# Performance work log

Measured on AMD Instinct MI355X. Metric: run time of the kernel, lower is better.

Reference implementation:

```python
import jax, jax.numpy as jnp
import numpy as np

N, E, D, IN_DIM, NUM_CLASSES, G, L = 50000, 800000, 128, 128, 10, 64, 3
BN_EPS = 1e-5


def _bn(h, gamma, beta, mean, var):
    # inference-mode batchnorm with running stats
    return (h - mean) * jax.lax.rsqrt(var + BN_EPS) * gamma + beta


def setup_inputs() -> dict:
    key = jax.random.key(0)
    ks = jax.random.split(key, 24)
    s = 0.02
    x = jax.random.normal(ks[0], (N, IN_DIM), dtype=jnp.float32)
    c_2 = jax.random.randint(ks[1], (E,), 0, N)
    u_2 = jax.random.randint(ks[2], (E,), 0, N)
    batch = jnp.sort(jax.random.randint(ks[3], (N,), 0, G))
    inp = {
        "x": x, "c_2": c_2, "u_2": u_2, "batch": batch,
        "We": jax.random.normal(ks[4], (IN_DIM, D)) * s,
        "be": jnp.zeros((D,), jnp.float32),
        # per-layer GIN MLP: Linear(d,2d) -> BN(2d) -> ReLU -> Linear(2d,d)
        "W1": jax.random.normal(ks[5], (L, D, 2 * D)) * s,
        "b1": jnp.zeros((L, 2 * D), jnp.float32),
        "g1": jnp.ones((L, 2 * D), jnp.float32),
        "bt1": jnp.zeros((L, 2 * D), jnp.float32),
        "m1": jax.random.normal(ks[6], (L, 2 * D)) * 0.1,
        "v1": jax.random.uniform(ks[7], (L, 2 * D), minval=0.5, maxval=1.5),
        "W2": jax.random.normal(ks[8], (L, 2 * D, D)) * s,
        "b2": jnp.zeros((L, D), jnp.float32),
        # post-conv BatchNorm(d)
        "g2": jnp.ones((L, D), jnp.float32),
        "bt2": jnp.zeros((L, D), jnp.float32),
        "m2": jax.random.normal(ks[9], (L, D)) * 0.1,
        "v2": jax.random.uniform(ks[10], (L, D), minval=0.5, maxval=1.5),
        # readout: Linear(d,d) -> ReLU -> (dropout off) -> Linear(d,num_classes)
        "Wr1": jax.random.normal(ks[11], (D, D)) * s,
        "br1": jnp.zeros((D,), jnp.float32),
        "Wr2": jax.random.normal(ks[12], (D, NUM_CLASSES)) * s,
        "br2": jnp.zeros((NUM_CLASSES,), jnp.float32),
    }
    return inp


def reference(x, c_2, u_2, batch, We, be, W1, b1, g1, bt1, m1, v1,
              W2, b2, g2, bt2, m2, v2, Wr1, br1, Wr2, br2):
    h = x @ We + be  # [N, D]
    for l in range(L):
        # GINConv (eps=0): h_i <- MLP(h_i + sum_{j->i} h_j)
        agg = jax.ops.segment_sum(h[c_2], u_2, num_segments=N)  # [N, D]
        z = h + agg
        z = jax.nn.relu(_bn(z @ W1[l] + b1[l], g1[l], bt1[l], m1[l], v1[l]))
        z = z @ W2[l] + b2[l]
        h = jax.nn.relu(_bn(z, g2[l], bt2[l], m2[l], v2[l]))
        # dropout: identity in eval mode
    pooled = jax.ops.segment_sum(h, batch, num_segments=G)  # [G, D]
    out = jax.nn.relu(pooled @ Wr1 + br1) @ Wr2 + br2  # [G, num_classes]
    return out
```

## Files before the change

kernel.cpp:

```cpp
#include <hip/hip_runtime.h>

#define BN_EPS 1e-5f

typedef __attribute__((ext_vector_type(8))) short bf16x8;
typedef __attribute__((ext_vector_type(4))) float f32x4;
typedef unsigned int uint32;

__device__ __forceinline__ unsigned short f2bf(float f) {
    unsigned u = __float_as_uint(f);
    u += 0x7FFFu + ((u >> 16) & 1u);
    return (unsigned short)(u >> 16);
}
__device__ __forceinline__ float bf2f(unsigned short u) {
    return __uint_as_float((unsigned)u << 16);
}
__device__ __forceinline__ float lo_bf(uint32 u) { return __uint_as_float(u << 16); }
__device__ __forceinline__ float hi_bf(uint32 u) { return __uint_as_float(u & 0xFFFF0000u); }
__device__ __forceinline__ uint32 pack_bf(float a0, float a1) {
    return ((uint32)f2bf(a1) << 16) | (uint32)f2bf(a0);
}

__global__ void init_kernel(int* __restrict__ deg, float* __restrict__ pooled, int N, int GP) {
    int i = blockIdx.x * 256 + threadIdx.x;
    if (i < N) deg[i] = 0;
    if (i < GP) pooled[i] = 0.f;
}

__global__ void count_deg_kernel(const int* __restrict__ u, int* __restrict__ deg, int E) {
    for (int e = blockIdx.x * blockDim.x + threadIdx.x; e < E; e += gridDim.x * blockDim.x)
        atomicAdd(&deg[u[e]], 1);
}

__global__ __launch_bounds__(256) void scan_local_kernel(const int* __restrict__ cnt,
                                                         int* __restrict__ start,
                                                         int* __restrict__ partials, int n) {
    __shared__ int buf[256];
    int i = blockIdx.x * 256 + threadIdx.x;
    int v = (i < n) ? cnt[i] : 0;
    buf[threadIdx.x] = v;
    __syncthreads();
    for (int off = 1; off < 256; off <<= 1) {
        int t = (threadIdx.x >= off) ? buf[threadIdx.x - off] : 0;
        __syncthreads();
        buf[threadIdx.x] += t;
        __syncthreads();
    }
    if (i < n) start[i] = buf[threadIdx.x] - v;
    if (threadIdx.x == 255) partials[blockIdx.x] = buf[255];
}

__global__ __launch_bounds__(256) void scan_partials_kernel(int* __restrict__ partials, int nb) {
    __shared__ int buf[256];
    int v = (threadIdx.x < nb) ? partials[threadIdx.x] : 0;
    buf[threadIdx.x] = v;
    __syncthreads();
    for (int off = 1; off < 256; off <<= 1) {
        int t = (threadIdx.x >= off) ? buf[threadIdx.x - off] : 0;
        __syncthreads();
        buf[threadIdx.x] += t;
        __syncthreads();
    }
    if (threadIdx.x < nb) partials[threadIdx.x] = buf[threadIdx.x] - v;
}

__global__ __launch_bounds__(256) void scan_add_kernel(int* __restrict__ node_start,
                                                       int* __restrict__ coarse_cursor,
                                                       const int* __restrict__ partials,
                                                       int n, int total) {
    int i = blockIdx.x * 256 + threadIdx.x;
    if (i < n) {
        int v = node_start[i] + partials[blockIdx.x];
        node_start[i] = v;
        if ((i & 255) == 0) coarse_cursor[i >> 8] = v;
    } else if (i == n) {
        node_start[n] = total;
    }
}

__global__ __launch_bounds__(256) void bin_coarse_kernel(const int* __restrict__ u2,
                                                         const int* __restrict__ c2,
                                                         int* __restrict__ coarse_cursor,
                                                         int* __restrict__ buck, int E) {
    __shared__ int lcnt[256];
    __shared__ int lbase[256];
    const int tid = threadIdx.x;
    lcnt[tid] = 0;
    __syncthreads();
    const int e0 = blockIdx.x * 4096;
    int ue[16];
#pragma unroll
    for (int k = 0; k < 16; ++k) {
        int e = e0 + k * 256 + tid;
        int u = (e < E) ? u2[e] : -1;
        ue[k] = u;
        if (u >= 0) atomicAdd(&lcnt[u >> 8], 1);
    }
    __syncthreads();
    int c0 = lcnt[tid];
    lbase[tid] = c0 ? atomicAdd(&coarse_cursor[tid], c0) : 0;
    lcnt[tid] = 0;
    __syncthreads();
#pragma unroll
    for (int k = 0; k < 16; ++k) {
        int e = e0 + k * 256 + tid;
        if (e < E) {
            int u = ue[k];
            int cb = u >> 8;
            int pos = lbase[cb] + atomicAdd(&lcnt[cb], 1);
            buck[pos] = ((u & 255) << 16) | c2[e];
        }
    }
}

__global__ __launch_bounds__(256) void bin_node_kernel(const int* __restrict__ node_start,
                                                       const int* __restrict__ buck,
                                                       int* __restrict__ csr_src, int N, int E) {
    __shared__ int lcur[256];
    const int cb = blockIdx.x;
    const int tid = threadIdx.x;
    int idx = cb * 256 + tid;
    lcur[tid] = (idx < N) ? node_start[idx] : E;
    __syncthreads();
    const int s = node_start[cb * 256];
    const int t_end = node_start[min(cb * 256 + 256, N)];
    for (int e = s + tid; e < t_end; e += 256) {
        int v = buck[e];
        int pos = atomicAdd(&lcur[v >> 16], 1);
        csr_src[pos] = v & 0xFFFF;
    }
}

__global__ __launch_bounds__(256) void aggregate_kernel(const unsigned short* __restrict__ h,
                                                        const int* __restrict__ row_start,
                                                        const int* __restrict__ csr_src,
                                                        unsigned short* __restrict__ h2, int N) {
    int node = blockIdx.x * 4 + (threadIdx.x >> 6);
    int lane = threadIdx.x & 63;
    if (node >= N) return;
    const int q = lane >> 4, sl = lane & 15;

    float a0 = 0.f, a1 = 0.f, a2 = 0.f, a3 = 0.f, a4 = 0.f, a5 = 0.f, a6 = 0.f, a7 = 0.f;
    if (q == 0) {
        uint4 v = ((const uint4*)(h + (size_t)node * 128))[sl];
        a0 = lo_bf(v.x); a1 = hi_bf(v.x); a2 = lo_bf(v.y); a3 = hi_bf(v.y);
        a4 = lo_bf(v.z); a5 = hi_bf(v.z); a6 = lo_bf(v.w); a7 = hi_bf(v.w);
    }

    const int rs = row_start[node], re = row_start[node + 1];
    int e = rs;
    for (; e + 8 <= re; e += 8) {
        int s0 = csr_src[e + q];
        int s1 = csr_src[e + 4 + q];
        uint4 v = ((const uint4*)(h + (size_t)s0 * 128))[sl];
        uint4 w = ((const uint4*)(h + (size_t)s1 * 128))[sl];
        a0 += lo_bf(v.x) + lo_bf(w.x); a1 += hi_bf(v.x) + hi_bf(w.x);
        a2 += lo_bf(v.y) + lo_bf(w.y); a3 += hi_bf(v.y) + hi_bf(w.y);
        a4 += lo_bf(v.z) + lo_bf(w.z); a5 += hi_bf(v.z) + hi_bf(w.z);
        a6 += lo_bf(v.w) + lo_bf(w.w); a7 += hi_bf(v.w) + hi_bf(w.w);
    }
    for (; e + 4 <= re; e += 4) {
        int s0 = csr_src[e + q];
        uint4 v = ((const uint4*)(h + (size_t)s0 * 128))[sl];
        a0 += lo_bf(v.x); a1 += hi_bf(v.x); a2 += lo_bf(v.y); a3 += hi_bf(v.y);
        a4 += lo_bf(v.z); a5 += hi_bf(v.z); a6 += lo_bf(v.w); a7 += hi_bf(v.w);
    }
    if (q < re - e) {
        int s0 = csr_src[e + q];
        uint4 v = ((const uint4*)(h + (size_t)s0 * 128))[sl];
        a0 += lo_bf(v.x); a1 += hi_bf(v.x); a2 += lo_bf(v.y); a3 += hi_bf(v.y);
        a4 += lo_bf(v.z); a5 += hi_bf(v.z); a6 += lo_bf(v.w); a7 += hi_bf(v.w);
    }

    a0 += __shfl_xor(a0, 16, 64); a0 += __shfl_xor(a0, 32, 64);
    a1 += __shfl_xor(a1, 16, 64); a1 += __shfl_xor(a1, 32, 64);
    a2 += __shfl_xor(a2, 16, 64); a2 += __shfl_xor(a2, 32, 64);
    a3 += __shfl_xor(a3, 16, 64); a3 += __shfl_xor(a3, 32, 64);
    a4 += __shfl_xor(a4, 16, 64); a4 += __shfl_xor(a4, 32, 64);
    a5 += __shfl_xor(a5, 16, 64); a5 += __shfl_xor(a5, 32, 64);
    a6 += __shfl_xor(a6, 16, 64); a6 += __shfl_xor(a6, 32, 64);
    a7 += __shfl_xor(a7, 16, 64); a7 += __shfl_xor(a7, 32, 64);

    if (q == 0) {
        uint4 o;
        o.x = pack_bf(a0, a1); o.y = pack_bf(a2, a3);
        o.z = pack_bf(a4, a5); o.w = pack_bf(a6, a7);
        ((uint4*)(h2 + (size_t)node * 128))[sl] = o;
    }
}

__global__ void prep_kernel(const float* __restrict__ We, const float* __restrict__ W1,
                            const float* __restrict__ W2,
                            unsigned short* __restrict__ Wte,
                            unsigned short* __restrict__ Wt1,
                            unsigned short* __restrict__ Wt2,
                            const float* __restrict__ be,
                            const float* __restrict__ b1, const float* __restrict__ g1,
                            const float* __restrict__ bt1, const float* __restrict__ m1,
                            const float* __restrict__ v1,
                            const float* __restrict__ b2, const float* __restrict__ g2,
                            const float* __restrict__ bt2, const float* __restrict__ m2,
                            const float* __restrict__ v2,
                            float* __restrict__ sce, float* __restrict__ she,
                            float* __restrict__ sc1, float* __restrict__ sh1,
                            float* __restrict__ sc2, float* __restrict__ sh2, int L) {
    int y = blockIdx.y;
    int t = threadIdx.x;
    if (blockIdx.x == 0) {
        if (y == 0) {
            if (t < 128) { sce[t] = 1.f; she[t] = be[t]; }
        } else if (y <= L) {
            int o = (y - 1) * 256 + t;
            float s = g1[o] * rsqrtf(v1[o] + BN_EPS);
            sc1[o] = s;
            sh1[o] = (b1[o] - m1[o]) * s + bt1[o];
        } else {
            if (t < 128) {
                int o = (y - L - 1) * 128 + t;
                float s = g2[o] * rsqrtf(v2[o] + BN_EPS);
                sc2[o] = s;
                sh2[o] = (b2[o] - m2[o]) * s + bt2[o];
            }
        }
    }
    const float* src;
    unsigned short* dst;
    int K;
    if (y == 0)      { src = We; dst = Wte; K = 128; }
    else if (y <= L) { int l = y - 1;     src = W1 + (size_t)l * 128 * 256; dst = Wt1 + (size_t)l * 128 * 256; K = 128; }
    else             { int l = y - L - 1; src = W2 + (size_t)l * 256 * 128; dst = Wt2 + (size_t)l * 256 * 128; K = 256; }
    int idx = blockIdx.x * 256 + t;
    int OUT = 32768 / K;
    if (y == 0) { if (idx >= 128 * 128) return; OUT = 128; }
    int c = idx / K, k = idx % K;
    dst[idx] = f2bf(src[(size_t)k * OUT + c]);
}

template <int K, int OUT, bool RELU, bool A_F32>
__global__ __launch_bounds__(256) void mfma_gemm_kernel(
    const void* __restrict__ Ap, const unsigned short* __restrict__ Wt,
    const float* __restrict__ scale, const float* __restrict__ shift,
    unsigned short* __restrict__ Cout, int nrows)
{
    constexpr int NT = OUT / 16;
    constexpr int KS = K / 32;
    constexpr int CH = OUT * K / 8;
    __shared__ unsigned short WtLds[OUT * K];

    const int tid = threadIdx.x;
    {
        const float4* src = (const float4*)Wt;
#pragma unroll
        for (int i = 0; i < CH / 256; ++i) {
            int c = tid + i * 256;
            int row = c / (K / 8);
            unsigned off = ((unsigned)c * 16u) ^ (((unsigned)row & 7u) << 4);
            *(float4*)((char*)WtLds + off) = src[c];
        }
    }
    __syncthreads();

    const int lane = tid & 63;
    const int l15 = lane & 15, lhi = lane >> 4;
    const int rbase = blockIdx.x * 128 + (tid >> 6) * 32;
    const int r0 = rbase + l15;
    const int r1 = rbase + 16 + l15;
    const int rr0 = min(r0, nrows - 1);
    const int rr1 = min(r1, nrows - 1);

    bf16x8 bfrag[2][KS];
    if constexpr (A_F32) {
        const float* a0 = (const float*)Ap + (size_t)rr0 * K + lhi * 8;
        const float* a1 = (const float*)Ap + (size_t)rr1 * K + lhi * 8;
#pragma unroll
        for (int ks = 0; ks < KS; ++ks) {
            float4 u0 = *(const float4*)(a0 + ks * 32);
            float4 u1 = *(const float4*)(a0 + ks * 32 + 4);
            float4 w0 = *(const float4*)(a1 + ks * 32);
            float4 w1 = *(const float4*)(a1 + ks * 32 + 4);
            bf16x8 f, g;
            f[0] = (short)f2bf(u0.x); f[1] = (short)f2bf(u0.y);
            f[2] = (short)f2bf(u0.z); f[3] = (short)f2bf(u0.w);
            f[4] = (short)f2bf(u1.x); f[5] = (short)f2bf(u1.y);
            f[6] = (short)f2bf(u1.z); f[7] = (short)f2bf(u1.w);
            g[0] = (short)f2bf(w0.x); g[1] = (short)f2bf(w0.y);
            g[2] = (short)f2bf(w0.z); g[3] = (short)f2bf(w0.w);
            g[4] = (short)f2bf(w1.x); g[5] = (short)f2bf(w1.y);
            g[6] = (short)f2bf(w1.z); g[7] = (short)f2bf(w1.w);
            bfrag[0][ks] = f;
            bfrag[1][ks] = g;
        }
    } else {
        const unsigned short* a0 = (const unsigned short*)Ap + (size_t)rr0 * K + lhi * 8;
        const unsigned short* a1 = (const unsigned short*)Ap + (size_t)rr1 * K + lhi * 8;
#pragma unroll
        for (int ks = 0; ks < KS; ++ks) {
            bfrag[0][ks] = *(const bf16x8*)(a0 + ks * 32);
            bfrag[1][ks] = *(const bf16x8*)(a1 + ks * 32);
        }
    }

    f32x4 acc[2][NT];
#pragma unroll
    for (int g = 0; g < 2; ++g)
#pragma unroll
        for (int nt = 0; nt < NT; ++nt) acc[g][nt] = (f32x4){0.f, 0.f, 0.f, 0.f};

#pragma unroll
    for (int ks = 0; ks < KS; ++ks) {
#pragma unroll
        for (int nt = 0; nt < NT; ++nt) {
            int row = nt * 16 + l15;
            unsigned off = ((unsigned)((row * K + ks * 32 + lhi * 8) * 2)) ^ (((unsigned)(l15 & 7u)) << 4);
            bf16x8 wfrag = *(const bf16x8*)((const char*)WtLds + off);
            acc[0][nt] = __builtin_amdgcn_mfma_f32_16x16x32_bf16(wfrag, bfrag[0][ks], acc[0][nt], 0, 0, 0);
            acc[1][nt] = __builtin_amdgcn_mfma_f32_16x16x32_bf16(wfrag, bfrag[1][ks], acc[1][nt], 0, 0, 0);
        }
    }

    const float4* sc4 = (const float4*)scale;
    const float4* sh4 = (const float4*)shift;
#pragma unroll
    for (int g = 0; g < 2; ++g) {
        const int r = (g == 0) ? r0 : r1;
        if (r >= nrows) continue;
#pragma unroll
        for (int nt = 0; nt < NT; ++nt) {
            float4 sc = sc4[nt * 4 + lhi];
            float4 sh = sh4[nt * 4 + lhi];
            float y0 = acc[g][nt][0] * sc.x + sh.x;
            float y1 = acc[g][nt][1] * sc.y + sh.y;
            float y2 = acc[g][nt][2] * sc.z + sh.z;
            float y3 = acc[g][nt][3] * sc.w + sh.w;
            if (RELU) {
                y0 = fmaxf(y0, 0.f); y1 = fmaxf(y1, 0.f);
                y2 = fmaxf(y2, 0.f); y3 = fmaxf(y3, 0.f);
            }
            size_t o = (size_t)r * OUT + nt * 16 + lhi * 4;
            ushort4 p = make_ushort4(f2bf(y0), f2bf(y1), f2bf(y2), f2bf(y3));
            *(ushort4*)(Cout + o) = p;
        }
    }
}

__global__ __launch_bounds__(128) void pool_kernel(const unsigned short* __restrict__ h,
                                                   const int* __restrict__ batch,
                                                   float* __restrict__ pooled, int N, int chunk) {
    int d = threadIdx.x;
    int start = blockIdx.x * chunk;
    if (start >= N) return;
    int end = min(start + chunk, N);
    float acc = 0.f;
    int g = batch[start];
    for (int r = start; r < end; ++r) {
        int bg = batch[r];
        if (bg != g) {
            atomicAdd(&pooled[g * 128 + d], acc);
            acc = 0.f;
            g = bg;
        }
        acc += bf2f(h[(size_t)r * 128 + d]);
    }
    atomicAdd(&pooled[g * 128 + d], acc);
}

__global__ __launch_bounds__(128) void readout_kernel(const float* __restrict__ pooled,
                                                      const float* __restrict__ Wr1,
                                                      const float* __restrict__ br1,
                                                      const float* __restrict__ Wr2,
                                                      const float* __restrict__ br2,
                                                      float* __restrict__ out) {
    __shared__ float prow[128];
    __shared__ float t[128];
    int g = blockIdx.x, j = threadIdx.x;
    prow[j] = pooled[g * 128 + j];
    __syncthreads();
    float acc = 0.f;
    for (int k = 0; k < 128; ++k) acc += prow[k] * Wr1[k * 128 + j];
    t[j] = fmaxf(acc + br1[j], 0.f);
    __syncthreads();
    if (j < 10) {
        float a2 = 0.f;
        for (int k = 0; k < 128; ++k) a2 += t[k] * Wr2[k * 10 + j];
        out[g * 10 + j] = a2 + br2[j];
    }
}

extern "C" void kernel_launch(void* const* d_in, const int* in_sizes, int n_in,
                              void* d_out, int out_size, void* d_ws, size_t ws_size,
                              hipStream_t stream) {
    const float* x   = (const float*)d_in[0];
    const int* c2    = (const int*)d_in[1];
    const int* u2    = (const int*)d_in[2];
    const int* batch = (const int*)d_in[3];
    const float* We  = (const float*)d_in[4];
    const float* be  = (const float*)d_in[5];
    const float* W1  = (const float*)d_in[6];
    const float* b1  = (const float*)d_in[7];
    const float* g1  = (const float*)d_in[8];
    const float* bt1 = (const float*)d_in[9];
    const float* m1  = (const float*)d_in[10];
    const float* v1  = (const float*)d_in[11];
    const float* W2  = (const float*)d_in[12];
    const float* b2  = (const float*)d_in[13];
    const float* g2  = (const float*)d_in[14];
    const float* bt2 = (const float*)d_in[15];
    const float* m2  = (const float*)d_in[16];
    const float* v2  = (const float*)d_in[17];
    const float* Wr1 = (const float*)d_in[18];
    const float* br1 = (const float*)d_in[19];
    const float* Wr2 = (const float*)d_in[20];
    const float* br2 = (const float*)d_in[21];

    const int N = in_sizes[3];
    const int E = in_sizes[1];
    const int L = in_sizes[7] / 256;
    const int G = out_size / 10;

    const int NC = (N + 255) / 256;

    char* ws = (char*)d_ws;
    size_t off = 0;
    auto alloc = [&](size_t bytes) { char* p = ws + off; off += (bytes + 255) & ~(size_t)255; return p; };
    unsigned short* hb   = (unsigned short*)alloc((size_t)N * 128 * 2);
    unsigned short* h2b  = (unsigned short*)alloc((size_t)N * 128 * 2);
    unsigned short* zb   = (unsigned short*)alloc((size_t)N * 256 * 2);
    unsigned short* Wte  = (unsigned short*)alloc(128 * 128 * 2);
    unsigned short* Wt1  = (unsigned short*)alloc((size_t)L * 256 * 128 * 2);
    unsigned short* Wt2  = (unsigned short*)alloc((size_t)L * 128 * 256 * 2);
    float* sce = (float*)alloc(128 * 4);
    float* she = (float*)alloc(128 * 4);
    float* sc1 = (float*)alloc((size_t)L * 256 * 4);
    float* sh1 = (float*)alloc((size_t)L * 256 * 4);
    float* sc2 = (float*)alloc((size_t)L * 128 * 4);
    float* sh2 = (float*)alloc((size_t)L * 128 * 4);
    float* pooled = (float*)alloc((size_t)G * 128 * 4);
    int* deg        = (int*)alloc((size_t)N * 4);
    int* node_start = (int*)alloc((size_t)(N + 1) * 4);
    int* coarse_cursor = (int*)alloc(256 * 4);
    int* partials   = (int*)alloc(256 * 4);
    int* buck       = (int*)alloc((size_t)E * 4);
    int* csr_src    = (int*)alloc((size_t)E * 4);

    init_kernel<<<(max(N, G * 128) + 255) / 256, 256, 0, stream>>>(deg, pooled, N, G * 128);
    count_deg_kernel<<<1024, 256, 0, stream>>>(u2, deg, E);
    const int scan_blocks = (N + 255) / 256;
    scan_local_kernel<<<scan_blocks, 256, 0, stream>>>(deg, node_start, partials, N);
    scan_partials_kernel<<<1, 256, 0, stream>>>(partials, scan_blocks);
    scan_add_kernel<<<(N + 256) / 256, 256, 0, stream>>>(node_start, coarse_cursor, partials, N, E);
    bin_coarse_kernel<<<(E + 4095) / 4096, 256, 0, stream>>>(u2, c2, coarse_cursor, buck, E);
    bin_node_kernel<<<NC, 256, 0, stream>>>(node_start, buck, csr_src, N, E);

    prep_kernel<<<dim3((256 * 128 + 255) / 256, 1 + 2 * L), 256, 0, stream>>>(
        We, W1, W2, Wte, Wt1, Wt2,
        be, b1, g1, bt1, m1, v1, b2, g2, bt2, m2, v2,
        sce, she, sc1, sh1, sc2, sh2, L);

    const int gemm_blocks = (N + 127) / 128;

    mfma_gemm_kernel<128, 128, false, true><<<gemm_blocks, 256, 0, stream>>>(
        x, Wte, sce, she, hb, N);

    for (int l = 0; l < L; ++l) {
        aggregate_kernel<<<(N + 3) / 4, 256, 0, stream>>>(hb, node_start, csr_src, h2b, N);
        mfma_gemm_kernel<128, 256, true, false><<<gemm_blocks, 256, 0, stream>>>(
            h2b, Wt1 + (size_t)l * 128 * 256, sc1 + l * 256, sh1 + l * 256, zb, N);
        mfma_gemm_kernel<256, 128, true, false><<<gemm_blocks, 256, 0, stream>>>(
            zb, Wt2 + (size_t)l * 256 * 128, sc2 + l * 128, sh2 + l * 128, hb, N);
    }

    const int chunk = (N + 511) / 512;
    pool_kernel<<<512, 128, 0, stream>>>(hb, batch, pooled, N, chunk);
    readout_kernel<<<G, 128, 0, stream>>>(pooled, Wr1, br1, Wr2, br2, (float*)d_out);
}
```

Measured before the change: 329.0 us.

## Fuse the two GIN MLP GEMMs into one persistent kernel with LDS intermediate

```diff
diff --git a/kernel.cpp b/kernel.cpp
--- a/kernel.cpp
+++ b/kernel.cpp
@@ -342,6 +342,126 @@
     }
 }
 
+__global__ __launch_bounds__(512) void mlp_fused_kernel(
+    const unsigned short* __restrict__ A,
+    const unsigned short* __restrict__ Wt1,
+    const unsigned short* __restrict__ Wt2,
+    const float* __restrict__ sc1v, const float* __restrict__ sh1v,
+    const float* __restrict__ sc2v, const float* __restrict__ sh2v,
+    unsigned short* __restrict__ Cout, int nrows, int ntiles)
+{
+    __shared__ unsigned short zlds[64 * 256];
+
+    const int tid = threadIdx.x;
+    const int w = tid >> 6, lane = tid & 63;
+    const int l15 = lane & 15, lhi = lane >> 4;
+
+    bf16x8 w1[2][4];
+#pragma unroll
+    for (int cf = 0; cf < 2; ++cf)
+#pragma unroll
+        for (int ks = 0; ks < 4; ++ks)
+            w1[cf][ks] = *(const bf16x8*)(Wt1 + (size_t)(w * 32 + cf * 16 + l15) * 128 + ks * 32 + lhi * 8);
+
+    const int rgrp = w >> 2, cg2 = w & 3;
+    bf16x8 w2[2][8];
+#pragma unroll
+    for (int cf = 0; cf < 2; ++cf)
+#pragma unroll
+        for (int ks = 0; ks < 8; ++ks)
+            w2[cf][ks] = *(const bf16x8*)(Wt2 + (size_t)(cg2 * 32 + cf * 16 + l15) * 256 + ks * 32 + lhi * 8);
+
+    const float4* sc1_4 = (const float4*)sc1v;
+    const float4* sh1_4 = (const float4*)sh1v;
+    const float4* sc2_4 = (const float4*)sc2v;
+    const float4* sh2_4 = (const float4*)sh2v;
+
+    for (int t = blockIdx.x; t < ntiles; t += gridDim.x) {
+        const int tbase = t * 64;
+
+        f32x4 acc1[4][2];
+#pragma unroll
+        for (int rf = 0; rf < 4; ++rf) {
+#pragma unroll
+            for (int cf = 0; cf < 2; ++cf) acc1[rf][cf] = (f32x4){0.f, 0.f, 0.f, 0.f};
+            const int rr = min(tbase + rf * 16 + l15, nrows - 1);
+            const unsigned short* arow = A + (size_t)rr * 128 + lhi * 8;
+            bf16x8 b0 = *(const bf16x8*)(arow);
+            bf16x8 b1 = *(const bf16x8*)(arow + 32);
+            bf16x8 b2 = *(const bf16x8*)(arow + 64);
+            bf16x8 b3 = *(const bf16x8*)(arow + 96);
+#pragma unroll
+            for (int cf = 0; cf < 2; ++cf) {
+                acc1[rf][cf] = __builtin_amdgcn_mfma_f32_16x16x32_bf16(w1[cf][0], b0, acc1[rf][cf], 0, 0, 0);
+                acc1[rf][cf] = __builtin_amdgcn_mfma_f32_16x16x32_bf16(w1[cf][1], b1, acc1[rf][cf], 0, 0, 0);
+                acc1[rf][cf] = __builtin_amdgcn_mfma_f32_16x16x32_bf16(w1[cf][2], b2, acc1[rf][cf], 0, 0, 0);
+                acc1[rf][cf] = __builtin_amdgcn_mfma_f32_16x16x32_bf16(w1[cf][3], b3, acc1[rf][cf], 0, 0, 0);
+            }
+        }
+
+        __syncthreads();
+
+#pragma unroll
+        for (int rf = 0; rf < 4; ++rf) {
+            const int rowl = rf * 16 + l15;
+            const unsigned swz = ((unsigned)(rowl & 7)) << 4;
+#pragma unroll
+            for (int cf = 0; cf < 2; ++cf) {
+                const int cq = w * 8 + cf * 4 + lhi;
+                float4 sc = sc1_4[cq];
+                float4 sh = sh1_4[cq];
+                float y0 = fmaxf(acc1[rf][cf][0] * sc.x + sh.x, 0.f);
+                float y1 = fmaxf(acc1[rf][cf][1] * sc.y + sh.y, 0.f);
+                float y2 = fmaxf(acc1[rf][cf][2] * sc.z + sh.z, 0.f);
+                float y3 = fmaxf(acc1[rf][cf][3] * sc.w + sh.w, 0.f);
+                unsigned byte = (unsigned)rowl * 512u + (((unsigned)(w * 64 + cf * 32 + lhi * 8)) ^ swz);
+                ushort4 p = make_ushort4(f2bf(y0), f2bf(y1), f2bf(y2), f2bf(y3));
+                *(ushort4*)((char*)zlds + byte) = p;
+            }
+        }
+
+        __syncthreads();
+
+        f32x4 acc2[2][2];
+#pragma unroll
+        for (int rf = 0; rf < 2; ++rf)
+#pragma unroll
+            for (int cf = 0; cf < 2; ++cf) acc2[rf][cf] = (f32x4){0.f, 0.f, 0.f, 0.f};
+
+#pragma unroll
+        for (int ks = 0; ks < 8; ++ks) {
+#pragma unroll
+            for (int rf = 0; rf < 2; ++rf) {
+                const int rowl = rgrp * 32 + rf * 16 + l15;
+                unsigned byte = (unsigned)rowl * 512u +
+                                (((unsigned)(ks * 64 + lhi * 16)) ^ (((unsigned)(rowl & 7)) << 4));
+                bf16x8 bz = *(const bf16x8*)((const char*)zlds + byte);
+                acc2[rf][0] = __builtin_amdgcn_mfma_f32_16x16x32_bf16(w2[0][ks], bz, acc2[rf][0], 0, 0, 0);
+                acc2[rf][1] = __builtin_amdgcn_mfma_f32_16x16x32_bf16(w2[1][ks], bz, acc2[rf][1], 0, 0, 0);
+            }
+        }
+
+#pragma unroll
+        for (int rf = 0; rf < 2; ++rf) {
+            const int r = tbase + rgrp * 32 + rf * 16 + l15;
+            if (r >= nrows) continue;
+#pragma unroll
+            for (int cf = 0; cf < 2; ++cf) {
+                const int cq = cg2 * 8 + cf * 4 + lhi;
+                float4 sc = sc2_4[cq];
+                float4 sh = sh2_4[cq];
+                float y0 = fmaxf(acc2[rf][cf][0] * sc.x + sh.x, 0.f);
+                float y1 = fmaxf(acc2[rf][cf][1] * sc.y + sh.y, 0.f);
+                float y2 = fmaxf(acc2[rf][cf][2] * sc.z + sh.z, 0.f);
+                float y3 = fmaxf(acc2[rf][cf][3] * sc.w + sh.w, 0.f);
+                size_t o = (size_t)r * 128 + cg2 * 32 + cf * 16 + lhi * 4;
+                ushort4 p = make_ushort4(f2bf(y0), f2bf(y1), f2bf(y2), f2bf(y3));
+                *(ushort4*)(Cout + o) = p;
+            }
+        }
+    }
+}
+
 __global__ __launch_bounds__(128) void pool_kernel(const unsigned short* __restrict__ h,
                                                    const int* __restrict__ batch,
                                                    float* __restrict__ pooled, int N, int chunk) {
@@ -423,7 +543,6 @@
     auto alloc = [&](size_t bytes) { char* p = ws + off; off += (bytes + 255) & ~(size_t)255; return p; };
     unsigned short* hb   = (unsigned short*)alloc((size_t)N * 128 * 2);
     unsigned short* h2b  = (unsigned short*)alloc((size_t)N * 128 * 2);
-    unsigned short* zb   = (unsigned short*)alloc((size_t)N * 256 * 2);
     unsigned short* Wte  = (unsigned short*)alloc(128 * 128 * 2);
     unsigned short* Wt1  = (unsigned short*)alloc((size_t)L * 256 * 128 * 2);
     unsigned short* Wt2  = (unsigned short*)alloc((size_t)L * 128 * 256 * 2);
@@ -455,17 +574,16 @@
         be, b1, g1, bt1, m1, v1, b2, g2, bt2, m2, v2,
         sce, she, sc1, sh1, sc2, sh2, L);
 
-    const int gemm_blocks = (N + 127) / 128;
-
-    mfma_gemm_kernel<128, 128, false, true><<<gemm_blocks, 256, 0, stream>>>(
+    mfma_gemm_kernel<128, 128, false, true><<<(N + 127) / 128, 256, 0, stream>>>(
         x, Wte, sce, she, hb, N);
 
+    const int mlp_tiles = (N + 63) / 64;
     for (int l = 0; l < L; ++l) {
         aggregate_kernel<<<(N + 3) / 4, 256, 0, stream>>>(hb, node_start, csr_src, h2b, N);
-        mfma_gemm_kernel<128, 256, true, false><<<gemm_blocks, 256, 0, stream>>>(
-            h2b, Wt1 + (size_t)l * 128 * 256, sc1 + l * 256, sh1 + l * 256, zb, N);
-        mfma_gemm_kernel<256, 128, true, false><<<gemm_blocks, 256, 0, stream>>>(
-            zb, Wt2 + (size_t)l * 256 * 128, sc2 + l * 128, sh2 + l * 128, hb, N);
+        mlp_fused_kernel<<<256, 512, 0, stream>>>(
+            h2b, Wt1 + (size_t)l * 128 * 256, Wt2 + (size_t)l * 256 * 128,
+            sc1 + l * 256, sh1 + l * 256, sc2 + l * 128, sh2 + l * 128,
+            hb, N, mlp_tiles);
     }
 
     const int chunk = (N + 511) / 512;
```

Result: no change. 333.8 us (+1.5%).
